# Optimization experiments

Hardware: AMD Instinct MI355X
Metric: run time of the kernel (lower is better)

## Reference

```python
import jax, jax.numpy as jnp
import numpy as np

N = 50000      # nodes
E = 800000     # edges (avg degree 16)
H = 256        # h_size
MAXCTX = 8     # max_context


def setup_inputs() -> dict:
    key = jax.random.key(0)
    ks = jax.random.split(key, 6)
    x = jax.random.normal(ks[0], (N, H), jnp.float32)
    edge_index = jax.random.randint(ks[1], (2, E), 0, N)
    node_label = jax.random.randint(ks[2], (N, MAXCTX), 0, N)
    context_len = jax.random.randint(ks[3], (N,), 0, MAXCTX)
    gcn_W = jax.random.normal(ks[4], (H, H), jnp.float32) / np.sqrt(H)
    gcn_b = jnp.zeros((H,), jnp.float32)
    resize_W = jax.random.normal(ks[5], (H * MAXCTX, H), jnp.float32) / np.sqrt(H * MAXCTX)
    resize_b = jnp.zeros((H,), jnp.float32)
    return {"x": x, "edge_index": edge_index, "node_label": node_label,
            "context_len": context_len, "gcn_W": gcn_W, "gcn_b": gcn_b,
            "resize_W": resize_W, "resize_b": resize_b}


def gcn_conv(x, edge_index, W, b, n):
    # PyG GCNConv: add self-loops, symmetric deg^-1/2 normalization, then linear.
    loop = jnp.arange(n)
    src = jnp.concatenate([edge_index[0], loop])
    dst = jnp.concatenate([edge_index[1], loop])
    deg = jax.ops.segment_sum(jnp.ones_like(dst, x.dtype), dst, num_segments=n)
    inv_sqrt = jax.lax.rsqrt(jnp.maximum(deg, 1.0))  # deg>=1 due to self-loops
    h = x @ W                                        # [n, H]
    coef = inv_sqrt[src] * inv_sqrt[dst]             # [E+n]
    out = jax.ops.segment_sum(h[src] * coef[:, None], dst, num_segments=n)
    return out + b


def reference(x, edge_index, node_label, context_len, gcn_W, gcn_b, resize_W, resize_b):
    n = x.shape[0]
    # gcn_layers=2: relu(GCN(x)) (dropout is identity in eval) then GCN again.
    feat = jax.nn.relu(gcn_conv(x, edge_index, gcn_W, gcn_b, n))
    feat = gcn_conv(feat, edge_index, gcn_W, gcn_b, n)
    # Batched variable-length context gather with zero padding.
    ctx = feat[node_label]                                            # [n, MAXCTX, H]
    mask = (jnp.arange(node_label.shape[1])[None, :] < context_len[:, None])
    ctx = ctx * mask[:, :, None].astype(feat.dtype)
    ctx = ctx.reshape(n, -1) @ resize_W + resize_b                    # [n, H]
    return feat * ctx                                                 # rep_vec per node
```

## Files before the change

kernel.cpp:

```cpp
#include <hip/hip_runtime.h>

typedef _Float16 f16;
typedef _Float16 f16x8 __attribute__((ext_vector_type(8)));
typedef float f32x16 __attribute__((ext_vector_type(16)));

#define MFMA(a, b, c) __builtin_amdgcn_mfma_f32_32x32x16_f16(a, b, c, 0, 0, 0)

__device__ __forceinline__ void gload_lds16(const f16* g, f16* l) {
    __builtin_amdgcn_global_load_lds(
        (const __attribute__((address_space(1))) unsigned int*)g,
        (__attribute__((address_space(3))) unsigned int*)l, 16, 0, 0);
}


#define NBMAX 256
#define CHUNK 8192
#define CAP   8192

__global__ __launch_bounds__(256) void bin_count(
        const int* __restrict__ dst, const int* __restrict__ clen,
        int* __restrict__ gbc, int* __restrict__ ghist, int E, int n, int chn) {
    __shared__ int bc[NBMAX];
    __shared__ int ch[9];
    int tid = threadIdx.x;
    bc[tid] = 0;
    if (tid < 9) ch[tid] = 0;
    __syncthreads();
    int e0 = blockIdx.x * CHUNK, e1 = min(e0 + CHUNK, E);
    for (int i = e0 + tid; i < e1; i += 256)
        atomicAdd(&bc[dst[i] >> 8], 1);
    int n0 = blockIdx.x * chn, n1 = min(n0 + chn, n);
    for (int i = n0 + tid; i < n1; i += 256) {
        int l = clen[i]; l = max(0, min(8, l));
        atomicAdd(&ch[l], 1);
    }
    __syncthreads();
    if (bc[tid]) atomicAdd(&gbc[tid], bc[tid]);
    if (tid < 9 && ch[tid]) atomicAdd(&ghist[tid], ch[tid]);
}

__global__ __launch_bounds__(256) void scan_small(
        const int* __restrict__ gbc, int* __restrict__ gbase,
        const int* __restrict__ ghist, int* __restrict__ chbase, int nb, int E) {
    __shared__ int s[NBMAX];
    int tid = threadIdx.x;
    int v = (tid < nb) ? gbc[tid] : 0;
    s[tid] = v;
    __syncthreads();
    for (int off = 1; off < 256; off <<= 1) {
        int u = (tid >= off) ? s[tid - off] : 0;
        __syncthreads();
        s[tid] += u;
        __syncthreads();
    }
    if (tid <= nb) gbase[tid] = (tid < nb) ? s[tid] - v : E;
    if (tid == 0) {
        int run = 0;
        for (int i = 0; i < 9; ++i) { int c = ghist[i]; chbase[i] = run; run += c; }
    }
}

__global__ __launch_bounds__(256) void bin_scatter(
        const int* __restrict__ src, const int* __restrict__ dst,
        const int* __restrict__ clen,
        const int* __restrict__ gbase, int* __restrict__ gfill,
        const int* __restrict__ chbase, int* __restrict__ chfill,
        int2* __restrict__ binned, int* __restrict__ perm, int* __restrict__ plen,
        int E, int n, int chn) {
    __shared__ int bc[NBMAX], bb[NBMAX];
    __shared__ int cc[9], cb[9];
    int tid = threadIdx.x;
    bc[tid] = 0;
    if (tid < 9) cc[tid] = 0;
    __syncthreads();
    int e0 = blockIdx.x * CHUNK, e1 = min(e0 + CHUNK, E);
    for (int i = e0 + tid; i < e1; i += 256)
        atomicAdd(&bc[dst[i] >> 8], 1);
    int n0 = blockIdx.x * chn, n1 = min(n0 + chn, n);
    for (int i = n0 + tid; i < n1; i += 256) {
        int l = clen[i]; l = max(0, min(8, l));
        atomicAdd(&cc[l], 1);
    }
    __syncthreads();
    {
        int c = bc[tid];
        bb[tid] = c ? gbase[tid] + atomicAdd(&gfill[tid], c) : 0;
        bc[tid] = 0;
    }
    if (tid < 9) {
        int c = cc[tid];
        cb[tid] = c ? chbase[tid] + atomicAdd(&chfill[tid], c) : 0;
        cc[tid] = 0;
    }
    __syncthreads();
    for (int i = e0 + tid; i < e1; i += 256) {
        int d = dst[i], b = d >> 8;
        int p = bb[b] + atomicAdd(&bc[b], 1);
        binned[p] = make_int2(src[i], d);
    }
    for (int i = n0 + tid; i < n1; i += 256) {
        int l = clen[i]; l = max(0, min(8, l));
        int p = cb[l] + atomicAdd(&cc[l], 1);
        perm[p] = i;
        plen[p] = l;
    }
}

__global__ __launch_bounds__(256) void csr_build(
        const int2* __restrict__ binned, const int* __restrict__ gbase,
        int* __restrict__ row_ptr, float* __restrict__ inv_s,
        int* __restrict__ ew, int E, int n) {
    __shared__ int cnt[256], base[256], fill[256];
    __shared__ int ebuf[CAP];
    int tid = threadIdx.x, b = blockIdx.x;
    int e0 = gbase[b], e1 = gbase[b + 1], sz = e1 - e0;
    cnt[tid] = 0;
    __syncthreads();
    for (int i = e0 + tid; i < e1; i += 256)
        atomicAdd(&cnt[binned[i].y & 255], 1);
    __syncthreads();
    int v = cnt[tid];
    base[tid] = v;
    __syncthreads();
    for (int off = 1; off < 256; off <<= 1) {
        int u = (tid >= off) ? base[tid - off] : 0;
        __syncthreads();
        base[tid] += u;
        __syncthreads();
    }
    int ex = base[tid] - v;
    base[tid] = ex;
    fill[tid] = 0;
    int node = b * 256 + tid;
    if (node < n) {
        row_ptr[node] = e0 + ex;
        inv_s[node] = rsqrtf((float)(v + 1));
    }
    if (b == 0 && tid == 0) row_ptr[n] = E;
    __syncthreads();
    for (int i = e0 + tid; i < e1; i += 256) {
        int2 q = binned[i];
        int lo = q.y & 255;
        int p = base[lo] + atomicAdd(&fill[lo], 1);
        if (p < CAP) ebuf[p] = q.x; else ew[e0 + p] = q.x;
    }
    __syncthreads();
    int lim = min(sz, CAP);
    for (int p = tid; p < lim; p += 256) ew[e0 + p] = ebuf[p];
}

__global__ __launch_bounds__(256) void pre_trans(
        const float* __restrict__ gW, f16* __restrict__ Wth, f16* __restrict__ Wtl,
        const float* __restrict__ rW, f16* __restrict__ Rth, f16* __restrict__ Rtl) {
    int b = blockIdx.x;
    __shared__ f16 Th[64][68], Tl[64][68];
    const float* src; f16 *dh, *dl; int K, k0, n0;
    if (b < 128) { src = rW; dh = Rth; dl = Rtl; K = 2048; k0 = (b >> 2) * 64; n0 = (b & 3) * 64; }
    else { int bb = b - 128; src = gW; dh = Wth; dl = Wtl; K = 256; k0 = (bb >> 2) * 64; n0 = (bb & 3) * 64; }
    int c = threadIdx.x & 63, r0 = threadIdx.x >> 6;
    for (int rr = r0; rr < 64; rr += 4) {
        float v = src[(size_t)(k0 + rr) * 256 + n0 + c];
        f16 h = (f16)v;
        Th[rr][c] = h; Tl[rr][c] = (f16)(v - (float)h);
    }
    __syncthreads();
    int k = threadIdx.x & 63, nr0 = threadIdx.x >> 6;
    for (int nn = nr0; nn < 64; nn += 4) {
        size_t oidx = (size_t)(n0 + nn) * K + k0 + k;
        dh[oidx] = Th[k][nn];
        dl[oidx] = Tl[k][nn];
    }
}


union H4 { f16 f[4]; ushort4 u; };

__global__ __launch_bounds__(512, 4) void agg_split(const float* __restrict__ X,
        const int* __restrict__ ew, const int* __restrict__ rp,
        const float* __restrict__ invs, f16* __restrict__ ohi, f16* __restrict__ olo, int n) {
    __shared__ float part[4][256];
    int w = threadIdx.x >> 6, lane = threadIdx.x & 63;
    int local = w >> 1, half = w & 1;
    int node = blockIdx.x * 4 + local;
    bool active = node < n;
    float4 acc = make_float4(0.f, 0.f, 0.f, 0.f);
    float si = 0.f;
    if (active) {
        si = invs[node];
        int e0 = rp[node], e1 = rp[node + 1];
        int mid = e0 + ((e1 - e0 + 1) >> 1);
        int lo = half ? mid : e0;
        int hi = half ? e1 : mid;
        if (!half) {
            float4 a = *((const float4*)(X + (size_t)node * 256) + lane);
            acc = make_float4(a.x * si, a.y * si, a.z * si, a.w * si);
        }
        int e = lo;
        for (; e + 8 <= hi; e += 8) {
            int q[8]; float ws[8]; float4 v[8];
            #pragma unroll
            for (int u = 0; u < 8; ++u) q[u] = ew[e + u];
            #pragma unroll
            for (int u = 0; u < 8; ++u) ws[u] = invs[q[u]];
            #pragma unroll
            for (int u = 0; u < 8; ++u) v[u] = *((const float4*)(X + (size_t)q[u] * 256) + lane);
            #pragma unroll
            for (int u = 0; u < 8; ++u) {
                acc.x = fmaf(ws[u], v[u].x, acc.x); acc.y = fmaf(ws[u], v[u].y, acc.y);
                acc.z = fmaf(ws[u], v[u].z, acc.z); acc.w = fmaf(ws[u], v[u].w, acc.w);
            }
        }
        for (; e < hi; ++e) {
            int q = ew[e];
            float wq = invs[q];
            float4 v = *((const float4*)(X + (size_t)q * 256) + lane);
            acc.x = fmaf(wq, v.x, acc.x); acc.y = fmaf(wq, v.y, acc.y);
            acc.z = fmaf(wq, v.z, acc.z); acc.w = fmaf(wq, v.w, acc.w);
        }
    }
    if (half) *(float4*)&part[local][lane * 4] = acc;
    __syncthreads();
    if (!half && active) {
        float4 o = *(const float4*)&part[local][lane * 4];
        float v0 = si * (acc.x + o.x), v1 = si * (acc.y + o.y);
        float v2 = si * (acc.z + o.z), v3 = si * (acc.w + o.w);
        H4 hh, ll;
        f16 h;
        h = (f16)v0; hh.f[0] = h; ll.f[0] = (f16)(v0 - (float)h);
        h = (f16)v1; hh.f[1] = h; ll.f[1] = (f16)(v1 - (float)h);
        h = (f16)v2; hh.f[2] = h; ll.f[2] = (f16)(v2 - (float)h);
        h = (f16)v3; hh.f[3] = h; ll.f[3] = (f16)(v3 - (float)h);
        size_t off = (size_t)node * 256 + lane * 4;
        *(ushort4*)(ohi + off) = hh.u;
        *(ushort4*)(olo + off) = ll.u;
    }
}


__global__ __launch_bounds__(256, 4) void gemm_reg(
        const f16* __restrict__ Ahi, const f16* __restrict__ Alo,
        const f16* __restrict__ Wth, const f16* __restrict__ Wtl,
        const float* __restrict__ bias,
        float* __restrict__ Of32, f16* __restrict__ Ohi, f16* __restrict__ Olo,
        int M, int relu) {
    int tid = threadIdx.x, w = tid >> 6, lane = tid & 63;
    int row0 = blockIdx.x * 32;
    int m = lane & 31, kh = lane >> 5;

    int ar = row0 + m; if (ar >= M) ar = M - 1;
    const f16* pAh = Ahi + (size_t)ar * 256 + kh * 8;
    const f16* pAl = Alo + (size_t)ar * 256 + kh * 8;
    const f16* pBh[2]; const f16* pBl[2];
    #pragma unroll
    for (int t = 0; t < 2; ++t) {
        int nn = w * 64 + t * 32 + m;
        pBh[t] = Wth + (size_t)nn * 256 + kh * 8;
        pBl[t] = Wtl + (size_t)nn * 256 + kh * 8;
    }

    f32x16 acc[2] = {};
    #pragma unroll 4
    for (int k8 = 0; k8 < 16; ++k8) {
        f16x8 ah = *(const f16x8*)(pAh + k8 * 16);
        f16x8 al = *(const f16x8*)(pAl + k8 * 16);
        #pragma unroll
        for (int t = 0; t < 2; ++t) {
            f16x8 bh = *(const f16x8*)(pBh[t] + k8 * 16);
            f16x8 bl = *(const f16x8*)(pBl[t] + k8 * 16);
            acc[t] = MFMA(ah, bh, acc[t]);
            acc[t] = MFMA(ah, bl, acc[t]);
            acc[t] = MFMA(al, bh, acc[t]);
        }
    }

    #pragma unroll
    for (int t = 0; t < 2; ++t) {
        int col = w * 64 + t * 32 + m;
        float bv = bias[col];
        #pragma unroll
        for (int r = 0; r < 16; ++r) {
            int row = row0 + (r & 3) + 8 * (r >> 2) + 4 * kh;
            if (row < M) {
                float v = acc[t][r] + bv;
                if (relu) v = fmaxf(v, 0.f);
                size_t idx = (size_t)row * 256 + col;
                if (Of32) Of32[idx] = v;
                if (Ohi) {
                    f16 h = (f16)v;
                    Ohi[idx] = h; Olo[idx] = (f16)(v - (float)h);
                }
            }
        }
    }
}


__global__ __launch_bounds__(256) void ctx_gemm(
        const f16* __restrict__ fhi, const f16* __restrict__ flo,
        const int* __restrict__ perm, const int* __restrict__ plen,
        const int* __restrict__ label,
        const f16* __restrict__ Rth, const f16* __restrict__ Rtl,
        const float* __restrict__ rbias, float* __restrict__ out,
        const f16* __restrict__ zp, int M) {
    __shared__ __align__(16) f16 LA[2][2][4096];
    __shared__ int s_lbl[8][64];
    __shared__ int s_perm[64];
    __shared__ int s_max;
    int tid = threadIdx.x, w = tid >> 6, lane = tid & 63;
    int row0 = (int)(gridDim.x - 1 - blockIdx.x) * 64;
    int m = lane & 31, kh = lane >> 5;

    if (tid == 0) s_max = 0;
    __syncthreads();
    if (tid < 64) {
        int r = row0 + tid;
        int p = (r < M) ? perm[r] : -1;
        s_perm[tid] = p;
        int len = (r < M) ? plen[r] : 0;
        atomicMax(&s_max, len);
        int4 l0 = make_int4(-1, -1, -1, -1), l1 = l0;
        if (p >= 0) {
            l0 = *(const int4*)(label + (size_t)p * 8);
            l1 = *(const int4*)(label + (size_t)p * 8 + 4);
        }
        s_lbl[0][tid] = (0 < len) ? l0.x : -1;
        s_lbl[1][tid] = (1 < len) ? l0.y : -1;
        s_lbl[2][tid] = (2 < len) ? l0.z : -1;
        s_lbl[3][tid] = (3 < len) ? l0.w : -1;
        s_lbl[4][tid] = (4 < len) ? l1.x : -1;
        s_lbl[5][tid] = (5 < len) ? l1.y : -1;
        s_lbl[6][tid] = (6 < len) ? l1.z : -1;
        s_lbl[7][tid] = (7 < len) ? l1.w : -1;
    }
    __syncthreads();
    int T = s_max * 4;

    f32x16 acc[2][2] = {};

    if (T > 0) {
        #define STAGE(t_, b_)                                                     \
        {                                                                         \
            int j_ = (t_) >> 2, k0e_ = ((t_) & 3) * 64;                           \
            int lbl_ = s_lbl[j_][lane];                                           \
            _Pragma("unroll")                                                     \
            for (int q = 0; q < 4; ++q) {                                         \
                int o_ = w * 4 + q;                                               \
                int mat_ = o_ >> 3, k8_ = o_ & 7;                                 \
                const f16* base_ = mat_ ? flo : fhi;                              \
                const f16* g_ = (lbl_ >= 0)                                       \
                    ? base_ + (size_t)lbl_ * 256 + k0e_ + k8_ * 8 : zp;           \
                gload_lds16(g_, &LA[b_][mat_][(k8_ * 64) * 8]);                   \
            }                                                                     \
        }
        STAGE(0, 0);
        __syncthreads();
        for (int t = 0; t < T; ++t) {
            if (t + 1 < T) STAGE(t + 1, (t + 1) & 1);
            int b = t & 1;
            int j = t >> 2, k0e = (t & 3) * 64;
            const f16* pBh[2]; const f16* pBl[2];
            #pragma unroll
            for (int jt = 0; jt < 2; ++jt) {
                int nn = w * 64 + jt * 32 + m;
                size_t boff = (size_t)nn * 2048 + j * 256 + k0e + kh * 8;
                pBh[jt] = Rth + boff;
                pBl[jt] = Rtl + boff;
            }
            #pragma unroll
            for (int s = 0; s < 4; ++s) {
                int k8 = s * 2 + kh;
                f16x8 ah[2], al[2];
                #pragma unroll
                for (int i = 0; i < 2; ++i) {
                    ah[i] = *(const f16x8*)&LA[b][0][(k8 * 64 + i * 32 + m) * 8];
                    al[i] = *(const f16x8*)&LA[b][1][(k8 * 64 + i * 32 + m) * 8];
                }
                #pragma unroll
                for (int jt = 0; jt < 2; ++jt) {
                    f16x8 bh = *(const f16x8*)(pBh[jt] + s * 16);
                    f16x8 bl = *(const f16x8*)(pBl[jt] + s * 16);
                    #pragma unroll
                    for (int i = 0; i < 2; ++i) {
                        acc[i][jt] = MFMA(ah[i], bh, acc[i][jt]);
                        acc[i][jt] = MFMA(ah[i], bl, acc[i][jt]);
                        acc[i][jt] = MFMA(al[i], bh, acc[i][jt]);
                    }
                }
            }
            __syncthreads();
        }
        #undef STAGE
    }

    #pragma unroll
    for (int jt = 0; jt < 2; ++jt) {
        int col = w * 64 + jt * 32 + m;
        float rbv = rbias[col];
        #pragma unroll
        for (int i = 0; i < 2; ++i) {
            #pragma unroll
            for (int r = 0; r < 16; ++r) {
                int lr = i * 32 + (r & 3) + 8 * (r >> 2) + 4 * kh;
                int p = s_perm[lr];
                if (p >= 0) {
                    size_t idx = (size_t)p * 256 + col;
                    float f2 = (float)fhi[idx] + (float)flo[idx];
                    out[idx] = f2 * (acc[i][jt][r] + rbv);
                }
            }
        }
    }
}


extern "C" void kernel_launch(void* const* d_in, const int* in_sizes, int n_in,
                              void* d_out, int out_size, void* d_ws, size_t ws_size,
                              hipStream_t stream) {
    const float* x    = (const float*)d_in[0];
    const int*   edge = (const int*)d_in[1];
    const int*   lbl  = (const int*)d_in[2];
    const int*   clen = (const int*)d_in[3];
    const float* gW   = (const float*)d_in[4];
    const float* gb   = (const float*)d_in[5];
    const float* rW   = (const float*)d_in[6];
    const float* rb   = (const float*)d_in[7];

    const int N = in_sizes[3];
    const int E = in_sizes[1] / 2;

    char* ws = (char*)d_ws;
    size_t off = 0;
    auto take = [&](size_t bytes) -> char* {
        char* p = ws + off;
        off = (off + bytes + 255) & ~(size_t)255;
        return p;
    };
    int*   g_small  = (int*)take(1024 * sizeof(int));
    int*   g_bcnt   = g_small;
    int*   g_bbase  = g_small + 256;
    int*   g_bfill  = g_small + 520;
    int*   g_chist  = g_small + 776;
    int*   g_chbase = g_small + 792;
    int*   g_chfill = g_small + 808;
    int*   row_ptr = (int*)take((size_t)(N + 1) * sizeof(int));
    int*   ew      = (int*)take((size_t)E * sizeof(int));
    int*   perm    = (int*)take((size_t)N * sizeof(int));
    int*   plen    = (int*)take((size_t)N * sizeof(int));
    float* inv_s   = (float*)take((size_t)N * sizeof(float));
    f16*   zp      = (f16*)take(1024);
    f16*   Wth     = (f16*)take((size_t)256 * 256 * sizeof(f16));
    f16*   Wtl     = (f16*)take((size_t)256 * 256 * sizeof(f16));
    f16*   Rth     = (f16*)take((size_t)256 * 2048 * sizeof(f16));
    f16*   Rtl     = (f16*)take((size_t)256 * 2048 * sizeof(f16));
    f16*   Ahi     = (f16*)take((size_t)N * 256 * sizeof(f16));
    f16*   Alo     = (f16*)take((size_t)N * 256 * sizeof(f16));
    float* Y1      = (float*)take((size_t)N * 256 * sizeof(float));
    f16*   Fhi     = (f16*)take((size_t)N * 256 * sizeof(f16));
    f16*   Flo     = (f16*)take((size_t)N * 256 * sizeof(f16));
    int2*  binned  = (int2*)Y1;

    hipMemsetAsync(g_small, 0, 1024 * sizeof(int), stream);
    hipMemsetAsync(zp, 0, 1024, stream);

    int NB   = (N + 255) >> 8;
    int GBIN = (E + CHUNK - 1) / CHUNK;
    int CHN  = (N + GBIN - 1) / GBIN;

    bin_count<<<GBIN, 256, 0, stream>>>(edge + E, clen, g_bcnt, g_chist, E, N, CHN);
    scan_small<<<1, 256, 0, stream>>>(g_bcnt, g_bbase, g_chist, g_chbase, NB, E);
    bin_scatter<<<GBIN, 256, 0, stream>>>(edge, edge + E, clen, g_bbase, g_bfill,
                                          g_chbase, g_chfill, binned, perm, plen,
                                          E, N, CHN);
    csr_build<<<NB, 256, 0, stream>>>(binned, g_bbase, row_ptr, inv_s, ew, E, N);
    pre_trans<<<144, 256, 0, stream>>>(gW, Wth, Wtl, rW, Rth, Rtl);

    int gB32 = (N + 31) / 32;
    int gB64 = (N + 63) / 64;
    agg_split<<<(N + 3) / 4, 512, 0, stream>>>(x, ew, row_ptr, inv_s, Ahi, Alo, N);
    gemm_reg<<<gB32, 256, 0, stream>>>(Ahi, Alo, Wth, Wtl, gb, Y1, nullptr, nullptr, N, 1);
    agg_split<<<(N + 3) / 4, 512, 0, stream>>>(Y1, ew, row_ptr, inv_s, Ahi, Alo, N);
    gemm_reg<<<gB32, 256, 0, stream>>>(Ahi, Alo, Wth, Wtl, gb, nullptr, Fhi, Flo, N, 0);
    ctx_gemm<<<gB64, 256, 0, stream>>>(Fhi, Flo, perm, plen, lbl, Rth, Rtl,
                                       rb, (float*)d_out, zp, N);
}
```

Baseline: 739.0 us.

## Triple-buffer ctx_gemm LDS gather with prefetch-two and register-preloaded B fragments

The context GEMM goes from double to triple buffering of the gathered A tiles in LDS and issues the gather for step t+2 while step t computes. All B fragments for a step are loaded into registers up front, before the MFMA loop. The per-step __syncthreads is replaced by explicit vmcnt waits plus s_barrier, with sched_barriers to fix the instruction order. This is meant to hide gather latency behind the MFMAs, at the cost of more LDS and more registers, under a launch bound that asks for 3 blocks per CU.

```diff
diff --git a/kernel.cpp b/kernel.cpp
--- a/kernel.cpp
+++ b/kernel.cpp
@@ -295,14 +295,14 @@
 }
 
 
-__global__ __launch_bounds__(256) void ctx_gemm(
+__global__ __launch_bounds__(256, 3) void ctx_gemm(
         const f16* __restrict__ fhi, const f16* __restrict__ flo,
         const int* __restrict__ perm, const int* __restrict__ plen,
         const int* __restrict__ label,
         const f16* __restrict__ Rth, const f16* __restrict__ Rtl,
         const float* __restrict__ rbias, float* __restrict__ out,
         const f16* __restrict__ zp, int M) {
-    __shared__ __align__(16) f16 LA[2][2][4096];
+    __shared__ __align__(16) f16 LA[3][2][4096];
     __shared__ int s_lbl[8][64];
     __shared__ int s_perm[64];
     __shared__ int s_max;
@@ -353,19 +353,29 @@
             }                                                                     \
         }
         STAGE(0, 0);
-        __syncthreads();
+        if (T > 1) STAGE(1, 1);
+        asm volatile("s_waitcnt vmcnt(0)" ::: "memory");
+        __builtin_amdgcn_s_barrier();
+        __builtin_amdgcn_sched_barrier(0);
         for (int t = 0; t < T; ++t) {
-            if (t + 1 < T) STAGE(t + 1, (t + 1) & 1);
-            int b = t & 1;
+            int b = t % 3;
             int j = t >> 2, k0e = (t & 3) * 64;
-            const f16* pBh[2]; const f16* pBl[2];
+            f16x8 Bh[4][2], Bl[4][2];
             #pragma unroll
             for (int jt = 0; jt < 2; ++jt) {
                 int nn = w * 64 + jt * 32 + m;
                 size_t boff = (size_t)nn * 2048 + j * 256 + k0e + kh * 8;
-                pBh[jt] = Rth + boff;
-                pBl[jt] = Rtl + boff;
-            }
+                const f16* ph = Rth + boff;
+                const f16* pl = Rtl + boff;
+                #pragma unroll
+                for (int s = 0; s < 4; ++s) {
+                    Bh[s][jt] = *(const f16x8*)(ph + s * 16);
+                    Bl[s][jt] = *(const f16x8*)(pl + s * 16);
+                }
+            }
+            __builtin_amdgcn_sched_barrier(0);
+            if (t + 2 < T) STAGE(t + 2, (t + 2) % 3);
+            __builtin_amdgcn_sched_barrier(0);
             #pragma unroll
             for (int s = 0; s < 4; ++s) {
                 int k8 = s * 2 + kh;
@@ -377,17 +387,21 @@
                 }
                 #pragma unroll
                 for (int jt = 0; jt < 2; ++jt) {
-                    f16x8 bh = *(const f16x8*)(pBh[jt] + s * 16);
-                    f16x8 bl = *(const f16x8*)(pBl[jt] + s * 16);
                     #pragma unroll
                     for (int i = 0; i < 2; ++i) {
-                        acc[i][jt] = MFMA(ah[i], bh, acc[i][jt]);
-                        acc[i][jt] = MFMA(ah[i], bl, acc[i][jt]);
-                        acc[i][jt] = MFMA(al[i], bh, acc[i][jt]);
+                        acc[i][jt] = MFMA(ah[i], Bh[s][jt], acc[i][jt]);
+                        acc[i][jt] = MFMA(ah[i], Bl[s][jt], acc[i][jt]);
+                        acc[i][jt] = MFMA(al[i], Bh[s][jt], acc[i][jt]);
                     }
                 }
             }
-            __syncthreads();
+            if (t + 2 < T) {
+                asm volatile("s_waitcnt vmcnt(4)" ::: "memory");
+            } else {
+                asm volatile("s_waitcnt vmcnt(0)" ::: "memory");
+            }
+            __builtin_amdgcn_s_barrier();
+            __builtin_amdgcn_sched_barrier(0);
         }
         #undef STAGE
     }
```

New measurement: 746.2 us. Within noise of the previous version (+1.0%).

## Shrink ctx_gemm row tile to 32 with XOR-swizzled row-major LDS layout

Applied to the files above, without the earlier changes.

Cuts the ctx_gemm block tile from 64 to 32 rows, which doubles the grid and halves per-block LDS and accumulator registers. The staged A tile changes from k8-major to row-major with an XOR swizzle on the 16-byte slot, so each gather load pulls contiguous segments of one label's row and LDS reads avoid bank conflicts. Rows sorted by context length now fall into finer groups, so fewer padded steps run per block. In exchange, each B (resize weight) fragment streamed from global memory is reused across half as many rows, which doubles B traffic.

```diff
diff --git a/kernel.cpp b/kernel.cpp
--- a/kernel.cpp
+++ b/kernel.cpp
@@ -302,17 +302,17 @@
         const f16* __restrict__ Rth, const f16* __restrict__ Rtl,
         const float* __restrict__ rbias, float* __restrict__ out,
         const f16* __restrict__ zp, int M) {
-    __shared__ __align__(16) f16 LA[2][2][4096];
-    __shared__ int s_lbl[8][64];
-    __shared__ int s_perm[64];
+    __shared__ __align__(16) f16 LA[2][2][2048];
+    __shared__ int s_lbl[8][32];
+    __shared__ int s_perm[32];
     __shared__ int s_max;
     int tid = threadIdx.x, w = tid >> 6, lane = tid & 63;
-    int row0 = (int)(gridDim.x - 1 - blockIdx.x) * 64;
+    int row0 = (int)(gridDim.x - 1 - blockIdx.x) * 32;
     int m = lane & 31, kh = lane >> 5;
 
     if (tid == 0) s_max = 0;
     __syncthreads();
-    if (tid < 64) {
+    if (tid < 32) {
         int r = row0 + tid;
         int p = (r < M) ? perm[r] : -1;
         s_perm[tid] = p;
@@ -335,21 +335,23 @@
     __syncthreads();
     int T = s_max * 4;
 
-    f32x16 acc[2][2] = {};
+    f32x16 acc[2] = {};
 
     if (T > 0) {
         #define STAGE(t_, b_)                                                     \
         {                                                                         \
             int j_ = (t_) >> 2, k0e_ = ((t_) & 3) * 64;                           \
-            int lbl_ = s_lbl[j_][lane];                                           \
+            int rl_ = lane >> 3;                                                  \
+            int k8s_ = (lane & 7) ^ rl_;                                          \
             _Pragma("unroll")                                                     \
-            for (int q = 0; q < 4; ++q) {                                         \
-                int o_ = w * 4 + q;                                               \
-                int mat_ = o_ >> 3, k8_ = o_ & 7;                                 \
+            for (int q = 0; q < 2; ++q) {                                         \
+                int o_ = w * 2 + q;                                               \
+                int mat_ = o_ >> 2, rg_ = o_ & 3;                                 \
+                int lbl_ = s_lbl[j_][rg_ * 8 + rl_];                              \
                 const f16* base_ = mat_ ? flo : fhi;                              \
                 const f16* g_ = (lbl_ >= 0)                                       \
-                    ? base_ + (size_t)lbl_ * 256 + k0e_ + k8_ * 8 : zp;           \
-                gload_lds16(g_, &LA[b_][mat_][(k8_ * 64) * 8]);                   \
+                    ? base_ + (size_t)lbl_ * 256 + k0e_ + k8s_ * 8 : zp;          \
+                gload_lds16(g_, &LA[b_][mat_][rg_ * 512]);                        \
             }                                                                     \
         }
         STAGE(0, 0);
@@ -369,22 +371,16 @@
             #pragma unroll
             for (int s = 0; s < 4; ++s) {
                 int k8 = s * 2 + kh;
-                f16x8 ah[2], al[2];
-                #pragma unroll
-                for (int i = 0; i < 2; ++i) {
-                    ah[i] = *(const f16x8*)&LA[b][0][(k8 * 64 + i * 32 + m) * 8];
-                    al[i] = *(const f16x8*)&LA[b][1][(k8 * 64 + i * 32 + m) * 8];
-                }
+                int slot = (k8 ^ (m & 7)) * 8;
+                f16x8 ah = *(const f16x8*)&LA[b][0][m * 64 + slot];
+                f16x8 al = *(const f16x8*)&LA[b][1][m * 64 + slot];
                 #pragma unroll
                 for (int jt = 0; jt < 2; ++jt) {
                     f16x8 bh = *(const f16x8*)(pBh[jt] + s * 16);
                     f16x8 bl = *(const f16x8*)(pBl[jt] + s * 16);
-                    #pragma unroll
-                    for (int i = 0; i < 2; ++i) {
-                        acc[i][jt] = MFMA(ah[i], bh, acc[i][jt]);
-                        acc[i][jt] = MFMA(ah[i], bl, acc[i][jt]);
-                        acc[i][jt] = MFMA(al[i], bh, acc[i][jt]);
-                    }
+                    acc[jt] = MFMA(ah, bh, acc[jt]);
+                    acc[jt] = MFMA(ah, bl, acc[jt]);
+                    acc[jt] = MFMA(al, bh, acc[jt]);
                 }
             }
             __syncthreads();
@@ -397,16 +393,13 @@
         int col = w * 64 + jt * 32 + m;
         float rbv = rbias[col];
         #pragma unroll
-        for (int i = 0; i < 2; ++i) {
-            #pragma unroll
-            for (int r = 0; r < 16; ++r) {
-                int lr = i * 32 + (r & 3) + 8 * (r >> 2) + 4 * kh;
-                int p = s_perm[lr];
-                if (p >= 0) {
-                    size_t idx = (size_t)p * 256 + col;
-                    float f2 = (float)fhi[idx] + (float)flo[idx];
-                    out[idx] = f2 * (acc[i][jt][r] + rbv);
-                }
+        for (int r = 0; r < 16; ++r) {
+            int lr = (r & 3) + 8 * (r >> 2) + 4 * kh;
+            int p = s_perm[lr];
+            if (p >= 0) {
+                size_t idx = (size_t)p * 256 + col;
+                float f2 = (float)fhi[idx] + (float)flo[idx];
+                out[idx] = f2 * (acc[jt][r] + rbv);
             }
         }
     }
@@ -475,11 +468,10 @@
     pre_trans<<<144, 256, 0, stream>>>(gW, Wth, Wtl, rW, Rth, Rtl);
 
     int gB32 = (N + 31) / 32;
-    int gB64 = (N + 63) / 64;
     agg_split<<<(N + 3) / 4, 512, 0, stream>>>(x, ew, row_ptr, inv_s, Ahi, Alo, N);
     gemm_reg<<<gB32, 256, 0, stream>>>(Ahi, Alo, Wth, Wtl, gb, Y1, nullptr, nullptr, N, 1);
     agg_split<<<(N + 3) / 4, 512, 0, stream>>>(Y1, ew, row_ptr, inv_s, Ahi, Alo, N);
     gemm_reg<<<gB32, 256, 0, stream>>>(Ahi, Alo, Wth, Wtl, gb, nullptr, Fhi, Flo, N, 0);
-    ctx_gemm<<<gB64, 256, 0, stream>>>(Fhi, Flo, perm, plen, lbl, Rth, Rtl,
+    ctx_gemm<<<gB32, 256, 0, stream>>>(Fhi, Flo, perm, plen, lbl, Rth, Rtl,
                                        rb, (float*)d_out, zp, N);
 }
```

New measurement: 808.9 us. +9.5%, slower.
